# Optimization experiments

Hardware: AMD Instinct MI355X
Metric: run time of the kernel (lower is better)

The kernel has to match this reference:

```python
import jax, jax.numpy as jnp
import numpy as np

EPS = 1e-5

def layer_norm(x, w, b):
    mu = jnp.mean(x, axis=-1, keepdims=True)
    var = jnp.mean(jnp.square(x - mu), axis=-1, keepdims=True)
    return (x - mu) * jax.lax.rsqrt(var + EPS) * w + b

def setup_inputs() -> dict:
    key = jax.random.key(0)
    ks = jax.random.split(key, 10)
    B, S, E = 8, 1024, 512
    s = 1.0 / np.sqrt(E)
    return {
        "Zi_1_alpha_beta": jax.random.normal(ks[0], (B, S, E), jnp.float32),
        "Zi_1_alpha": jax.random.normal(ks[1], (B, S, E), jnp.float32),
        "ln_w": jnp.ones((E,), jnp.float32),
        "ln_b": jnp.zeros((E,), jnp.float32),
        "in_proj_w": jax.random.uniform(ks[2], (3 * E, E), jnp.float32, -s, s),
        "in_proj_b": jnp.zeros((3 * E,), jnp.float32),
        "out_proj_w": jax.random.uniform(ks[3], (E, E), jnp.float32, -s, s),
        "out_proj_b": jnp.zeros((E,), jnp.float32),
        "ff_w": jax.random.uniform(ks[4], (E, E), jnp.float32, -s, s),
        "ff_b": jax.random.uniform(ks[5], (E,), jnp.float32, -s, s),
    }

def reference(Zi_1_alpha_beta, Zi_1_alpha, ln_w, ln_b, in_proj_w, in_proj_b,
              out_proj_w, out_proj_b, ff_w, ff_b):
    B, Sq, E = Zi_1_alpha_beta.shape
    Sk = Zi_1_alpha.shape[1]
    H = 8
    dh = E // H

    q_in = layer_norm(Zi_1_alpha_beta, ln_w, ln_b)   # query source
    kv_in = layer_norm(Zi_1_alpha, ln_w, ln_b)       # key/value source

    Wq, Wk, Wv = in_proj_w[:E], in_proj_w[E:2 * E], in_proj_w[2 * E:]
    bq, bk, bv = in_proj_b[:E], in_proj_b[E:2 * E], in_proj_b[2 * E:]
    q = (q_in @ Wq.T + bq).reshape(B, Sq, H, dh)
    k = (kv_in @ Wk.T + bk).reshape(B, Sk, H, dh)
    v = (kv_in @ Wv.T + bv).reshape(B, Sk, H, dh)

    scale = 1.0 / np.sqrt(dh)
    scores = jnp.einsum('bqhd,bkhd->bhqk', q, k) * scale   # [B,H,Sq,Sk]
    attn = jax.nn.softmax(scores, axis=-1)
    ctx = jnp.einsum('bhqk,bkhd->bqhd', attn, v).reshape(B, Sq, E)
    attn_out = ctx @ out_proj_w.T + out_proj_b

    # torch MHA with need_weights=True averages weights over heads
    attn_weights = jnp.mean(attn, axis=1)  # [B,Sq,Sk]

    x = attn_out + Zi_1_alpha_beta
    x_n = layer_norm(x, ln_w, ln_b)
    ff = x_n @ ff_w.T + ff_b
    final = layer_norm(x_n + ff, ln_w, ln_b)
    return final, attn_weights
```

## Files before the change

### kernel.cpp

```cpp
#include <hip/hip_runtime.h>
#include <math.h>

#define EPS 1e-5f

constexpr int B = 8, S = 1024, E = 512, H = 8;
constexpr int M = B * S;

typedef __attribute__((ext_vector_type(8))) short short8;
typedef __attribute__((ext_vector_type(4))) float f32x4;

static __device__ __forceinline__ unsigned short f2bf(float f) {
    unsigned int x = __float_as_uint(f);
    x += 0x7FFFu + ((x >> 16) & 1u);
    return (unsigned short)(x >> 16);
}
static __device__ __forceinline__ float bf2f(unsigned short u) {
    return __uint_as_float(((unsigned int)u) << 16);
}

typedef __attribute__((address_space(3))) unsigned int  lds_uint;
typedef __attribute__((address_space(1))) unsigned int  glb_uint;
static __device__ __forceinline__ void gload16(const unsigned short* g, unsigned short* l) {
    __builtin_amdgcn_global_load_lds((const glb_uint*)g, (lds_uint*)l, 16, 0, 0);
}
template <int N>
static __device__ __forceinline__ void waitvm() {
    __builtin_amdgcn_s_waitcnt(0x0F70 | N);
}

__global__ __launch_bounds__(256) void prep_kernel(
    const float* __restrict__ wqkv, const float* __restrict__ wo,
    const float* __restrict__ wf, unsigned short* __restrict__ wout,
    const float* __restrict__ x0, const float* __restrict__ x1,
    const float* __restrict__ w, const float* __restrict__ bb,
    unsigned short* __restrict__ o0, unsigned short* __restrict__ o1) {
    const int bid = blockIdx.x;
    if (bid < 1280) {
        int base = (bid * 256 + threadIdx.x) * 4;
        float4 v;
        if (base < 3 * E * E)           v = *(const float4*)(wqkv + base);
        else if (base < 4 * E * E)      v = *(const float4*)(wo + (base - 3 * E * E));
        else                            v = *(const float4*)(wf + (base - 4 * E * E));
        ushort4 o;
        o.x = f2bf(v.x); o.y = f2bf(v.y); o.z = f2bf(v.z); o.w = f2bf(v.w);
        *(ushort4*)(wout + base) = o;
        return;
    }
    int row = (bid - 1280) * 4 + (threadIdx.x >> 6);
    int lane = threadIdx.x & 63;
    const float* x = row < M ? x0 : x1;
    unsigned short* out = row < M ? o0 : o1;
    int r = row < M ? row : row - M;
    const float* xr = x + (size_t)r * E + lane * 8;
    float4 v0 = *(const float4*)xr;
    float4 v1 = *(const float4*)(xr + 4);
    float vv[8] = {v0.x, v0.y, v0.z, v0.w, v1.x, v1.y, v1.z, v1.w};
    float s = 0.f;
    #pragma unroll
    for (int i = 0; i < 8; i++) s += vv[i];
    #pragma unroll
    for (int o = 1; o < 64; o <<= 1) s += __shfl_xor(s, o);
    float mu = s * (1.0f / E);
    float qs = 0.f;
    #pragma unroll
    for (int i = 0; i < 8; i++) { float d = vv[i] - mu; qs += d * d; }
    #pragma unroll
    for (int o = 1; o < 64; o <<= 1) qs += __shfl_xor(qs, o);
    float rs = rsqrtf(qs * (1.0f / E) + EPS);
    float4 w0 = *(const float4*)(w + lane * 8), w1 = *(const float4*)(w + lane * 8 + 4);
    float4 b0 = *(const float4*)(bb + lane * 8), b1 = *(const float4*)(bb + lane * 8 + 4);
    float ww[8] = {w0.x, w0.y, w0.z, w0.w, w1.x, w1.y, w1.z, w1.w};
    float bv[8] = {b0.x, b0.y, b0.z, b0.w, b1.x, b1.y, b1.z, b1.w};
    short8 o8;
    #pragma unroll
    for (int i = 0; i < 8; i++) o8[i] = (short)f2bf((vv[i] - mu) * rs * ww[i] + bv[i]);
    *(short8*)(out + (size_t)r * E + lane * 8) = o8;
}

__global__ __launch_bounds__(256) void ln_bf16_kernel(
    const float* __restrict__ x, const float* __restrict__ w,
    const float* __restrict__ bb, unsigned short* __restrict__ out) {
    int row = blockIdx.x * 4 + (threadIdx.x >> 6);
    int lane = threadIdx.x & 63;
    const float* xr = x + (size_t)row * E + lane * 8;
    float4 v0 = *(const float4*)xr;
    float4 v1 = *(const float4*)(xr + 4);
    float vv[8] = {v0.x, v0.y, v0.z, v0.w, v1.x, v1.y, v1.z, v1.w};
    float s = 0.f;
    #pragma unroll
    for (int i = 0; i < 8; i++) s += vv[i];
    #pragma unroll
    for (int o = 1; o < 64; o <<= 1) s += __shfl_xor(s, o);
    float mu = s * (1.0f / E);
    float qs = 0.f;
    #pragma unroll
    for (int i = 0; i < 8; i++) { float d = vv[i] - mu; qs += d * d; }
    #pragma unroll
    for (int o = 1; o < 64; o <<= 1) qs += __shfl_xor(qs, o);
    float rs = rsqrtf(qs * (1.0f / E) + EPS);
    float4 w0 = *(const float4*)(w + lane * 8), w1 = *(const float4*)(w + lane * 8 + 4);
    float4 b0 = *(const float4*)(bb + lane * 8), b1 = *(const float4*)(bb + lane * 8 + 4);
    float ww[8] = {w0.x, w0.y, w0.z, w0.w, w1.x, w1.y, w1.z, w1.w};
    float bv[8] = {b0.x, b0.y, b0.z, b0.w, b1.x, b1.y, b1.z, b1.w};
    short8 o8;
    #pragma unroll
    for (int i = 0; i < 8; i++) o8[i] = (short)f2bf((vv[i] - mu) * rs * ww[i] + bv[i]);
    *(short8*)(out + (size_t)row * E + lane * 8) = o8;
}

__global__ __launch_bounds__(256) void ln_full_kernel(
    const float* __restrict__ x, const float* __restrict__ w,
    const float* __restrict__ bb, float* __restrict__ out) {
    int row = blockIdx.x * 4 + (threadIdx.x >> 6);
    int lane = threadIdx.x & 63;
    const float* xr = x + (size_t)row * E + lane * 8;
    float4 v0 = *(const float4*)xr;
    float4 v1 = *(const float4*)(xr + 4);
    float vv[8] = {v0.x, v0.y, v0.z, v0.w, v1.x, v1.y, v1.z, v1.w};
    float s = 0.f;
    #pragma unroll
    for (int i = 0; i < 8; i++) s += vv[i];
    #pragma unroll
    for (int o = 1; o < 64; o <<= 1) s += __shfl_xor(s, o);
    float mu = s * (1.0f / E);
    float qs = 0.f;
    #pragma unroll
    for (int i = 0; i < 8; i++) { float d = vv[i] - mu; qs += d * d; }
    #pragma unroll
    for (int o = 1; o < 64; o <<= 1) qs += __shfl_xor(qs, o);
    float rs = rsqrtf(qs * (1.0f / E) + EPS);
    float4 w0 = *(const float4*)(w + lane * 8), w1 = *(const float4*)(w + lane * 8 + 4);
    float4 b0 = *(const float4*)(bb + lane * 8), b1 = *(const float4*)(bb + lane * 8 + 4);
    float* op = out + (size_t)row * E + lane * 8;
    float4 o0, o1;
    o0.x = (vv[0] - mu) * rs * w0.x + b0.x;
    o0.y = (vv[1] - mu) * rs * w0.y + b0.y;
    o0.z = (vv[2] - mu) * rs * w0.z + b0.z;
    o0.w = (vv[3] - mu) * rs * w0.w + b0.w;
    o1.x = (vv[4] - mu) * rs * w1.x + b1.x;
    o1.y = (vv[5] - mu) * rs * w1.y + b1.y;
    o1.z = (vv[6] - mu) * rs * w1.z + b1.z;
    o1.w = (vv[7] - mu) * rs * w1.w + b1.w;
    *(float4*)op = o0;
    *(float4*)(op + 4) = o1;
}

__global__ __launch_bounds__(256) void gemm_o_red(
    const unsigned short* __restrict__ A, const unsigned short* __restrict__ W,
    const float* __restrict__ bias, const float* __restrict__ residf,
    float* __restrict__ C0,
    const unsigned short* __restrict__ awp, float* __restrict__ aw) {
    __shared__ unsigned short As[64 * 32];
    __shared__ unsigned short Bs[128 * 32];
    const int bid = blockIdx.x;
    const int t = threadIdx.x;
    if (bid >= 512) {
        const size_t PLN = (size_t)B * S * S;
        size_t idx = ((size_t)(bid - 512) * 256 + t) * 8;
        float acc[8] = {};
        #pragma unroll
        for (int p = 0; p < 2; p++) {
            short8 v = *(const short8*)(awp + p * PLN + idx);
            #pragma unroll
            for (int j = 0; j < 8; j++) acc[j] += bf2f((unsigned short)v[j]);
        }
        float4 o0 = make_float4(acc[0] * (1.0f / H), acc[1] * (1.0f / H),
                                acc[2] * (1.0f / H), acc[3] * (1.0f / H));
        float4 o1 = make_float4(acc[4] * (1.0f / H), acc[5] * (1.0f / H),
                                acc[6] * (1.0f / H), acc[7] * (1.0f / H));
        *(float4*)(aw + idx) = o0;
        *(float4*)(aw + idx + 4) = o1;
        return;
    }
    const int wave = t >> 6, lane = t & 63;
    const int quad = lane >> 4, l16 = lane & 15;
    const int m0 = (bid & 127) * 64, n0 = (bid >> 7) * 128;
    const int wm = (wave >> 1) * 32, wn = (wave & 1) * 64;
    const int srow = t >> 2;
    const int skof = (t & 3) * 8;

    f32x4 acc[2][4];
    #pragma unroll
    for (int i = 0; i < 2; i++)
        #pragma unroll
        for (int j = 0; j < 4; j++) acc[i][j] = (f32x4){0.f, 0.f, 0.f, 0.f};

    for (int k0 = 0; k0 < E; k0 += 32) {
        gload16(A + (size_t)(m0 + srow) * E + k0 + skof,        As + t * 8);
        gload16(W + (size_t)(n0 + srow) * E + k0 + skof,        Bs + t * 8);
        gload16(W + (size_t)(n0 + 64 + srow) * E + k0 + skof,   Bs + 2048 + t * 8);
        __syncthreads();
        short8 af[2], bfr[4];
        #pragma unroll
        for (int i = 0; i < 2; i++)
            af[i] = *(const short8*)&As[(wm + i * 16 + l16) * 32 + quad * 8];
        #pragma unroll
        for (int j = 0; j < 4; j++)
            bfr[j] = *(const short8*)&Bs[(wn + j * 16 + l16) * 32 + quad * 8];
        #pragma unroll
        for (int i = 0; i < 2; i++)
            #pragma unroll
            for (int j = 0; j < 4; j++)
                acc[i][j] = __builtin_amdgcn_mfma_f32_16x16x32_bf16(af[i], bfr[j], acc[i][j], 0, 0, 0);
        __syncthreads();
    }

    #pragma unroll
    for (int i = 0; i < 2; i++) {
        const int mrow0 = m0 + wm + i * 16 + quad * 4;
        #pragma unroll
        for (int j = 0; j < 4; j++) {
            const int ncol = n0 + wn + j * 16 + l16;
            const float bval = bias[ncol];
            #pragma unroll
            for (int r = 0; r < 4; r++) {
                size_t idx = (size_t)(mrow0 + r) * 512 + ncol;
                C0[idx] = acc[i][j][r] + bval + residf[idx];
            }
        }
    }
}

__global__ __launch_bounds__(256) void gemm_mfma64_ff(
    const unsigned short* __restrict__ A, const unsigned short* __restrict__ W,
    const float* __restrict__ bias, const unsigned short* __restrict__ residb,
    float* __restrict__ C0) {
    __shared__ unsigned short As[64 * 32];
    __shared__ unsigned short Bs[128 * 32];
    const int t = threadIdx.x;
    const int wave = t >> 6, lane = t & 63;
    const int quad = lane >> 4, l16 = lane & 15;
    const int m0 = blockIdx.x * 64, n0 = blockIdx.y * 128;
    const int wm = (wave >> 1) * 32, wn = (wave & 1) * 64;
    const int srow = t >> 2;
    const int skof = (t & 3) * 8;

    f32x4 acc[2][4];
    #pragma unroll
    for (int i = 0; i < 2; i++)
        #pragma unroll
        for (int j = 0; j < 4; j++) acc[i][j] = (f32x4){0.f, 0.f, 0.f, 0.f};

    for (int k0 = 0; k0 < E; k0 += 32) {
        gload16(A + (size_t)(m0 + srow) * E + k0 + skof,        As + t * 8);
        gload16(W + (size_t)(n0 + srow) * E + k0 + skof,        Bs + t * 8);
        gload16(W + (size_t)(n0 + 64 + srow) * E + k0 + skof,   Bs + 2048 + t * 8);
        __syncthreads();
        short8 af[2], bfr[4];
        #pragma unroll
        for (int i = 0; i < 2; i++)
            af[i] = *(const short8*)&As[(wm + i * 16 + l16) * 32 + quad * 8];
        #pragma unroll
        for (int j = 0; j < 4; j++)
            bfr[j] = *(const short8*)&Bs[(wn + j * 16 + l16) * 32 + quad * 8];
        #pragma unroll
        for (int i = 0; i < 2; i++)
            #pragma unroll
            for (int j = 0; j < 4; j++)
                acc[i][j] = __builtin_amdgcn_mfma_f32_16x16x32_bf16(af[i], bfr[j], acc[i][j], 0, 0, 0);
        __syncthreads();
    }

    #pragma unroll
    for (int i = 0; i < 2; i++) {
        const int mrow0 = m0 + wm + i * 16 + quad * 4;
        #pragma unroll
        for (int j = 0; j < 4; j++) {
            const int ncol = n0 + wn + j * 16 + l16;
            const float bval = bias[ncol];
            #pragma unroll
            for (int r = 0; r < 4; r++) {
                size_t idx = (size_t)(mrow0 + r) * 512 + ncol;
                C0[idx] = acc[i][j][r] + bval + bf2f(residb[idx]);
            }
        }
    }
}

__global__ __launch_bounds__(256) void gemm_qkv(
    const unsigned short* __restrict__ Aq, const unsigned short* __restrict__ Akv,
    const unsigned short* __restrict__ W,
    const float* __restrict__ bias,
    unsigned short* __restrict__ qout,
    unsigned short* __restrict__ kout,
    unsigned short* __restrict__ vtout) {
    __shared__ unsigned short As[128 * 32];
    __shared__ unsigned short Bs[128 * 32];
    const int t = threadIdx.x;
    const int wave = t >> 6, lane = t & 63;
    const int quad = lane >> 4, l16 = lane & 15;
    const bool isq = blockIdx.y < 4;
    const int yy = isq ? blockIdx.y : blockIdx.y - 4;
    const unsigned short* A  = isq ? Aq : Akv;
    const unsigned short* Wb = W + (isq ? 0 : (size_t)E * E);
    const float* bb = bias + (isq ? 0 : E);
    const int m0 = blockIdx.x * 128, n0 = yy * 128;
    const int wm = (wave >> 1) * 64, wn = (wave & 1) * 64;

    const int srow = t >> 2;
    const int skof = (t & 3) * 8;

    f32x4 acc[4][4];
    #pragma unroll
    for (int i = 0; i < 4; i++)
        #pragma unroll
        for (int j = 0; j < 4; j++) acc[i][j] = (f32x4){0.f, 0.f, 0.f, 0.f};

    for (int k0 = 0; k0 < E; k0 += 32) {
        gload16(A + (size_t)(m0 + srow) * E + k0 + skof,         As + t * 8);
        gload16(A + (size_t)(m0 + 64 + srow) * E + k0 + skof,    As + 2048 + t * 8);
        gload16(Wb + (size_t)(n0 + srow) * E + k0 + skof,        Bs + t * 8);
        gload16(Wb + (size_t)(n0 + 64 + srow) * E + k0 + skof,   Bs + 2048 + t * 8);
        __syncthreads();
        short8 af[4], bfr[4];
        #pragma unroll
        for (int i = 0; i < 4; i++)
            af[i] = *(const short8*)&As[(wm + i * 16 + l16) * 32 + quad * 8];
        #pragma unroll
        for (int j = 0; j < 4; j++)
            bfr[j] = *(const short8*)&Bs[(wn + j * 16 + l16) * 32 + quad * 8];
        #pragma unroll
        for (int i = 0; i < 4; i++)
            #pragma unroll
            for (int j = 0; j < 4; j++)
                acc[i][j] = __builtin_amdgcn_mfma_f32_16x16x32_bf16(af[i], bfr[j], acc[i][j], 0, 0, 0);
        __syncthreads();
    }

    #pragma unroll
    for (int i = 0; i < 4; i++) {
        const int mrow0 = m0 + wm + i * 16 + quad * 4;
        #pragma unroll
        for (int j = 0; j < 4; j++) {
            const int ncol = n0 + wn + j * 16 + l16;
            const float bval = bb[ncol];
            if (isq) {
                #pragma unroll
                for (int r = 0; r < 4; r++)
                    qout[(size_t)(mrow0 + r) * 512 + ncol] = f2bf(acc[i][j][r] + bval);
            } else if (ncol < 512) {
                #pragma unroll
                for (int r = 0; r < 4; r++)
                    kout[(size_t)(mrow0 + r) * 512 + ncol] = f2bf(acc[i][j][r] + bval);
            } else {
                const int nv = ncol - 512;
                const int b2 = mrow0 >> 10, s0v = mrow0 & 1023;
                ushort4 o;
                o.x = f2bf(acc[i][j][0] + bval);
                o.y = f2bf(acc[i][j][1] + bval);
                o.z = f2bf(acc[i][j][2] + bval);
                o.w = f2bf(acc[i][j][3] + bval);
                *(ushort4*)(vtout + ((size_t)b2 * 512 + nv) * 1024 + s0v) = o;
            }
        }
    }
}

__global__ __launch_bounds__(256, 2) void attn_mfma_kernel(
    const unsigned short* __restrict__ q,
    const unsigned short* __restrict__ k,
    const unsigned short* __restrict__ vt,
    unsigned short* __restrict__ ctx,
    unsigned short* __restrict__ awp) {
    __shared__ unsigned short s_mem[16 * 1032];
    __shared__ unsigned short s_v[4 * 2048];
    __shared__ float s_red[2][4][16];

    const int t = threadIdx.x;
    const int wave = t >> 6, lane = t & 63;
    const int quad = lane >> 4, l16 = lane & 15;
    const int qt    = blockIdx.x >> 4;
    const int panel = blockIdx.x & 15;
    const int hg    = panel & 1;
    const int b     = panel >> 1;
    const int q0   = qt * 16;
    const size_t qrow = ((size_t)(b * S + q0 + l16)) * E;

    unsigned short* karea = s_mem + wave * 4128;
    unsigned short* varea = s_v + wave * 2048;

    const int dr = lane >> 3;
    const int dc = lane & 7;
    const int csrc = dc ^ dr;
    const int sw7 = l16 & 7;

    f32x4 awacc[16];
    #pragma unroll
    for (int i = 0; i < 16; i++) awacc[i] = (f32x4){0.f, 0.f, 0.f, 0.f};

    #pragma clang loop unroll(disable)
    for (int hh = 0; hh < 4; hh++) {
        const int h = hg * 4 + hh;

        auto stage_k = [&](int c, int buf) {
            const unsigned short* src =
                k + ((size_t)(b * S + wave * 256 + c * 32 + dr)) * E + h * 64 + csrc * 8;
            unsigned short* dst = karea + buf * 2048 + dr * 64 + dc * 8;
            gload16(src,                  dst);
            gload16(src + (size_t)8 * E,  dst + 512);
            gload16(src + (size_t)16 * E, dst + 1024);
            gload16(src + (size_t)24 * E, dst + 1536);
        };
        auto stage_v = [&](int cv, int buf) {
            const unsigned short* src =
                vt + ((size_t)(b * E + h * 64 + wave * 16 + dr)) * S + cv * 64 + csrc * 8;
            unsigned short* dst = varea + buf * 1024 + dr * 64 + dc * 8;
            gload16(src,                 dst);
            gload16(src + (size_t)8 * S, dst + 512);
        };

        short8 aq0 = *(const short8*)(q + qrow + h * 64 + quad * 8);
        short8 aq1 = *(const short8*)(q + qrow + h * 64 + 32 + quad * 8);

        f32x4 sacc[16];
        stage_k(0, 0);
        stage_k(1, 1);
        #pragma unroll
        for (int c = 0; c < 8; c++) {
            if (c < 7) waitvm<4>(); else waitvm<0>();
            const unsigned short* kbuf = karea + (c & 1) * 2048;
            #pragma unroll
            for (int ntl = 0; ntl < 2; ntl++) {
                const int rl = ntl * 16 + l16;
                short8 kf0 = *(const short8*)(kbuf + rl * 64 + ((quad)     ^ sw7) * 8);
                short8 kf1 = *(const short8*)(kbuf + rl * 64 + ((4 + quad) ^ sw7) * 8);
                f32x4 cc = (f32x4){0.f, 0.f, 0.f, 0.f};
                cc = __builtin_amdgcn_mfma_f32_16x16x32_bf16(aq0, kf0, cc, 0, 0, 0);
                cc = __builtin_amdgcn_mfma_f32_16x16x32_bf16(aq1, kf1, cc, 0, 0, 0);
                sacc[c * 2 + ntl] = cc * 0.125f;
            }
            if (c < 6) stage_k(c + 2, c & 1);
        }

        float lm[4], ls[4];
        #pragma unroll
        for (int r = 0; r < 4; r++) {
            float mv = sacc[0][r];
            #pragma unroll
            for (int nt = 1; nt < 16; nt++) mv = fmaxf(mv, sacc[nt][r]);
            #pragma unroll
            for (int o = 1; o < 16; o <<= 1) mv = fmaxf(mv, __shfl_xor(mv, o));
            lm[r] = mv;
            ls[r] = 0.f;
        }
        #pragma unroll
        for (int nt = 0; nt < 16; nt++)
            #pragma unroll
            for (int r = 0; r < 4; r++) {
                float e = __expf(sacc[nt][r] - lm[r]);
                sacc[nt][r] = e;
                ls[r] += e;
            }
        #pragma unroll
        for (int r = 0; r < 4; r++) {
            #pragma unroll
            for (int o = 1; o < 16; o <<= 1) ls[r] += __shfl_xor(ls[r], o);
        }
        if (l16 == 0) {
            #pragma unroll
            for (int r = 0; r < 4; r++) {
                s_red[0][wave][quad * 4 + r] = lm[r];
                s_red[1][wave][quad * 4 + r] = ls[r];
            }
        }
        __syncthreads();
        float scale[4];
        #pragma unroll
        for (int r = 0; r < 4; r++) {
            const int row = quad * 4 + r;
            float m0 = s_red[0][0][row], m1 = s_red[0][1][row];
            float m2 = s_red[0][2][row], m3 = s_red[0][3][row];
            float gmax = fmaxf(fmaxf(m0, m1), fmaxf(m2, m3));
            float gsum = s_red[1][0][row] * __expf(m0 - gmax)
                       + s_red[1][1][row] * __expf(m1 - gmax)
                       + s_red[1][2][row] * __expf(m2 - gmax)
                       + s_red[1][3][row] * __expf(m3 - gmax);
            scale[r] = __expf(lm[r] - gmax) / gsum;
        }

        #pragma unroll
        for (int nt = 0; nt < 16; nt++) {
            #pragma unroll
            for (int r = 0; r < 4; r++) {
                float p = sacc[nt][r] * scale[r];
                awacc[nt][r] += p;
                s_mem[(quad * 4 + r) * 1032 + wave * 256 + nt * 16 + l16] = f2bf(p);
            }
        }
        __syncthreads();

        f32x4 cacc0 = (f32x4){0.f, 0.f, 0.f, 0.f};
        f32x4 cacc1 = (f32x4){0.f, 0.f, 0.f, 0.f};
        stage_v(0, 0);
        stage_v(1, 1);
        #pragma unroll
        for (int cv = 0; cv < 16; cv++) {
            if (cv < 15) waitvm<2>(); else waitvm<0>();
            const unsigned short* vbuf = varea + (cv & 1) * 1024;
            short8 vf0 = *(const short8*)(vbuf + l16 * 64 + ((quad)     ^ sw7) * 8);
            short8 vf1 = *(const short8*)(vbuf + l16 * 64 + ((4 + quad) ^ sw7) * 8);
            short8 pf0 = *(const short8*)(s_mem + l16 * 1032 + cv * 64 + quad * 8);
            short8 pf1 = *(const short8*)(s_mem + l16 * 1032 + cv * 64 + 32 + quad * 8);
            cacc0 = __builtin_amdgcn_mfma_f32_16x16x32_bf16(pf0, vf0, cacc0, 0, 0, 0);
            cacc1 = __builtin_amdgcn_mfma_f32_16x16x32_bf16(pf1, vf1, cacc1, 0, 0, 0);
            if (cv < 14) stage_v(cv + 2, cv & 1);
        }
        f32x4 cacc = cacc0 + cacc1;
        unsigned short* crow = ctx + ((size_t)(b * S + q0)) * E + h * 64 + wave * 16 + l16;
        #pragma unroll
        for (int r = 0; r < 4; r++)
            crow[(size_t)(quad * 4 + r) * E] = f2bf(cacc[r]);
        __syncthreads();
    }

    #pragma unroll
    for (int nt = 0; nt < 16; nt++) {
        #pragma unroll
        for (int r = 0; r < 4; r++)
            awp[((size_t)((hg * B + b) * S + q0 + quad * 4 + r)) * S +
                wave * 256 + nt * 16 + l16] = f2bf(awacc[nt][r]);
    }
}

extern "C" void kernel_launch(void* const* d_in, const int* in_sizes, int n_in,
                              void* d_out, int out_size, void* d_ws, size_t ws_size,
                              hipStream_t stream) {
    const float* Zab  = (const float*)d_in[0];
    const float* Za   = (const float*)d_in[1];
    const float* lnw  = (const float*)d_in[2];
    const float* lnb  = (const float*)d_in[3];
    const float* Wqkv = (const float*)d_in[4];
    const float* bqkv = (const float*)d_in[5];
    const float* Wo   = (const float*)d_in[6];
    const float* bo   = (const float*)d_in[7];
    const float* Wf   = (const float*)d_in[8];
    const float* bf   = (const float*)d_in[9];

    float* out_final = (float*)d_out;
    float* out_aw    = out_final + (size_t)B * S * E;

    char* ws = (char*)d_ws;
    unsigned short* qb   = (unsigned short*)(ws);
    unsigned short* kb   = (unsigned short*)(ws + (8u << 20));
    unsigned short* vtb  = (unsigned short*)(ws + (16u << 20));
    unsigned short* ctxb = (unsigned short*)(ws + (24u << 20));
    unsigned short* aqb  = (unsigned short*)(ws + (32u << 20));
    unsigned short* akvb = (unsigned short*)(ws + (40u << 20));
    unsigned short* awp  = (unsigned short*)(ws + (32ull << 20));
    unsigned short* wbf  = (unsigned short*)(ws + (96ull << 20));
    float* xb  = (float*)(ws);
    float* tb  = (float*)(ws + (16u << 20));
    unsigned short* xnb = aqb;

    dim3 blk(256);

    prep_kernel<<<1280 + 4096, blk, 0, stream>>>(Wqkv, Wo, Wf, wbf,
                                                 Zab, Za, lnw, lnb, aqb, akvb);

    gemm_qkv<<<dim3(M / 128, 12), blk, 0, stream>>>(aqb, akvb, wbf, bqkv, qb, kb, vtb);

    attn_mfma_kernel<<<B * 2 * 64, blk, 0, stream>>>(qb, kb, vtb, ctxb, awp);

    gemm_o_red<<<512 + 4096, blk, 0, stream>>>(ctxb, wbf + (size_t)3*E*E, bo,
                                               Zab, xb, awp, out_aw);

    ln_bf16_kernel<<<M / 4, blk, 0, stream>>>(xb, lnw, lnb, xnb);

    gemm_mfma64_ff<<<dim3(M / 64, 4), blk, 0, stream>>>(xnb, wbf + (size_t)4*E*E, bf, xnb, tb);

    ln_full_kernel<<<M / 4, blk, 0, stream>>>(tb, lnw, lnb, out_final);
}
```

Baseline: 253.4 us.

## Fuse post-attention LayerNorm, FF GEMM and final LayerNorm into one kernel

```diff
diff --git a/kernel.cpp b/kernel.cpp
--- a/kernel.cpp
+++ b/kernel.cpp
@@ -77,74 +77,6 @@
     *(short8*)(out + (size_t)r * E + lane * 8) = o8;
 }
 
-__global__ __launch_bounds__(256) void ln_bf16_kernel(
-    const float* __restrict__ x, const float* __restrict__ w,
-    const float* __restrict__ bb, unsigned short* __restrict__ out) {
-    int row = blockIdx.x * 4 + (threadIdx.x >> 6);
-    int lane = threadIdx.x & 63;
-    const float* xr = x + (size_t)row * E + lane * 8;
-    float4 v0 = *(const float4*)xr;
-    float4 v1 = *(const float4*)(xr + 4);
-    float vv[8] = {v0.x, v0.y, v0.z, v0.w, v1.x, v1.y, v1.z, v1.w};
-    float s = 0.f;
-    #pragma unroll
-    for (int i = 0; i < 8; i++) s += vv[i];
-    #pragma unroll
-    for (int o = 1; o < 64; o <<= 1) s += __shfl_xor(s, o);
-    float mu = s * (1.0f / E);
-    float qs = 0.f;
-    #pragma unroll
-    for (int i = 0; i < 8; i++) { float d = vv[i] - mu; qs += d * d; }
-    #pragma unroll
-    for (int o = 1; o < 64; o <<= 1) qs += __shfl_xor(qs, o);
-    float rs = rsqrtf(qs * (1.0f / E) + EPS);
-    float4 w0 = *(const float4*)(w + lane * 8), w1 = *(const float4*)(w + lane * 8 + 4);
-    float4 b0 = *(const float4*)(bb + lane * 8), b1 = *(const float4*)(bb + lane * 8 + 4);
-    float ww[8] = {w0.x, w0.y, w0.z, w0.w, w1.x, w1.y, w1.z, w1.w};
-    float bv[8] = {b0.x, b0.y, b0.z, b0.w, b1.x, b1.y, b1.z, b1.w};
-    short8 o8;
-    #pragma unroll
-    for (int i = 0; i < 8; i++) o8[i] = (short)f2bf((vv[i] - mu) * rs * ww[i] + bv[i]);
-    *(short8*)(out + (size_t)row * E + lane * 8) = o8;
-}
-
-__global__ __launch_bounds__(256) void ln_full_kernel(
-    const float* __restrict__ x, const float* __restrict__ w,
-    const float* __restrict__ bb, float* __restrict__ out) {
-    int row = blockIdx.x * 4 + (threadIdx.x >> 6);
-    int lane = threadIdx.x & 63;
-    const float* xr = x + (size_t)row * E + lane * 8;
-    float4 v0 = *(const float4*)xr;
-    float4 v1 = *(const float4*)(xr + 4);
-    float vv[8] = {v0.x, v0.y, v0.z, v0.w, v1.x, v1.y, v1.z, v1.w};
-    float s = 0.f;
-    #pragma unroll
-    for (int i = 0; i < 8; i++) s += vv[i];
-    #pragma unroll
-    for (int o = 1; o < 64; o <<= 1) s += __shfl_xor(s, o);
-    float mu = s * (1.0f / E);
-    float qs = 0.f;
-    #pragma unroll
-    for (int i = 0; i < 8; i++) { float d = vv[i] - mu; qs += d * d; }
-    #pragma unroll
-    for (int o = 1; o < 64; o <<= 1) qs += __shfl_xor(qs, o);
-    float rs = rsqrtf(qs * (1.0f / E) + EPS);
-    float4 w0 = *(const float4*)(w + lane * 8), w1 = *(const float4*)(w + lane * 8 + 4);
-    float4 b0 = *(const float4*)(bb + lane * 8), b1 = *(const float4*)(bb + lane * 8 + 4);
-    float* op = out + (size_t)row * E + lane * 8;
-    float4 o0, o1;
-    o0.x = (vv[0] - mu) * rs * w0.x + b0.x;
-    o0.y = (vv[1] - mu) * rs * w0.y + b0.y;
-    o0.z = (vv[2] - mu) * rs * w0.z + b0.z;
-    o0.w = (vv[3] - mu) * rs * w0.w + b0.w;
-    o1.x = (vv[4] - mu) * rs * w1.x + b1.x;
-    o1.y = (vv[5] - mu) * rs * w1.y + b1.y;
-    o1.z = (vv[6] - mu) * rs * w1.z + b1.z;
-    o1.w = (vv[7] - mu) * rs * w1.w + b1.w;
-    *(float4*)op = o0;
-    *(float4*)(op + 4) = o1;
-}
-
 __global__ __launch_bounds__(256) void gemm_o_red(
     const unsigned short* __restrict__ A, const unsigned short* __restrict__ W,
     const float* __restrict__ bias, const float* __restrict__ residf,
@@ -221,59 +153,126 @@
     }
 }
 
-__global__ __launch_bounds__(256) void gemm_mfma64_ff(
-    const unsigned short* __restrict__ A, const unsigned short* __restrict__ W,
-    const float* __restrict__ bias, const unsigned short* __restrict__ residb,
-    float* __restrict__ C0) {
-    __shared__ unsigned short As[64 * 32];
-    __shared__ unsigned short Bs[128 * 32];
+__global__ __launch_bounds__(256) void ffn_fused_kernel(
+    const float* __restrict__ x,
+    const unsigned short* __restrict__ W,
+    const float* __restrict__ bias,
+    const float* __restrict__ lnw, const float* __restrict__ lnb,
+    float* __restrict__ out) {
+    __shared__ unsigned short Axn[16 * 520];
+    __shared__ unsigned short Bs[512 * 32];
+    __shared__ float s_red[2][4][16];
     const int t = threadIdx.x;
     const int wave = t >> 6, lane = t & 63;
     const int quad = lane >> 4, l16 = lane & 15;
-    const int m0 = blockIdx.x * 64, n0 = blockIdx.y * 128;
-    const int wm = (wave >> 1) * 32, wn = (wave & 1) * 64;
+    const int m0 = blockIdx.x * 16;
+
+    #pragma unroll
+    for (int rr = 0; rr < 4; rr++) {
+        const int row = wave * 4 + rr;
+        const float* xr = x + (size_t)(m0 + row) * E + lane * 8;
+        float4 v0 = *(const float4*)xr;
+        float4 v1 = *(const float4*)(xr + 4);
+        float vv[8] = {v0.x, v0.y, v0.z, v0.w, v1.x, v1.y, v1.z, v1.w};
+        float s = 0.f;
+        #pragma unroll
+        for (int i = 0; i < 8; i++) s += vv[i];
+        #pragma unroll
+        for (int o = 1; o < 64; o <<= 1) s += __shfl_xor(s, o);
+        float mu = s * (1.0f / E);
+        float qs = 0.f;
+        #pragma unroll
+        for (int i = 0; i < 8; i++) { float d = vv[i] - mu; qs += d * d; }
+        #pragma unroll
+        for (int o = 1; o < 64; o <<= 1) qs += __shfl_xor(qs, o);
+        float rs = rsqrtf(qs * (1.0f / E) + EPS);
+        float4 w0 = *(const float4*)(lnw + lane * 8), w1 = *(const float4*)(lnw + lane * 8 + 4);
+        float4 b0 = *(const float4*)(lnb + lane * 8), b1 = *(const float4*)(lnb + lane * 8 + 4);
+        float ww[8] = {w0.x, w0.y, w0.z, w0.w, w1.x, w1.y, w1.z, w1.w};
+        float bv[8] = {b0.x, b0.y, b0.z, b0.w, b1.x, b1.y, b1.z, b1.w};
+        short8 o8;
+        #pragma unroll
+        for (int i = 0; i < 8; i++) o8[i] = (short)f2bf((vv[i] - mu) * rs * ww[i] + bv[i]);
+        *(short8*)&Axn[row * 520 + lane * 8] = o8;
+    }
+    __syncthreads();
+
+    f32x4 acc[8];
+    #pragma unroll
+    for (int j = 0; j < 8; j++) acc[j] = (f32x4){0.f, 0.f, 0.f, 0.f};
     const int srow = t >> 2;
     const int skof = (t & 3) * 8;
-
-    f32x4 acc[2][4];
-    #pragma unroll
-    for (int i = 0; i < 2; i++)
-        #pragma unroll
-        for (int j = 0; j < 4; j++) acc[i][j] = (f32x4){0.f, 0.f, 0.f, 0.f};
-
+    #pragma clang loop unroll(disable)
     for (int k0 = 0; k0 < E; k0 += 32) {
-        gload16(A + (size_t)(m0 + srow) * E + k0 + skof,        As + t * 8);
-        gload16(W + (size_t)(n0 + srow) * E + k0 + skof,        Bs + t * 8);
-        gload16(W + (size_t)(n0 + 64 + srow) * E + k0 + skof,   Bs + 2048 + t * 8);
-        __syncthreads();
-        short8 af[2], bfr[4];
-        #pragma unroll
-        for (int i = 0; i < 2; i++)
-            af[i] = *(const short8*)&As[(wm + i * 16 + l16) * 32 + quad * 8];
-        #pragma unroll
-        for (int j = 0; j < 4; j++)
-            bfr[j] = *(const short8*)&Bs[(wn + j * 16 + l16) * 32 + quad * 8];
-        #pragma unroll
-        for (int i = 0; i < 2; i++)
-            #pragma unroll
-            for (int j = 0; j < 4; j++)
-                acc[i][j] = __builtin_amdgcn_mfma_f32_16x16x32_bf16(af[i], bfr[j], acc[i][j], 0, 0, 0);
-        __syncthreads();
-    }
-
-    #pragma unroll
-    for (int i = 0; i < 2; i++) {
-        const int mrow0 = m0 + wm + i * 16 + quad * 4;
-        #pragma unroll
-        for (int j = 0; j < 4; j++) {
-            const int ncol = n0 + wn + j * 16 + l16;
-            const float bval = bias[ncol];
-            #pragma unroll
-            for (int r = 0; r < 4; r++) {
-                size_t idx = (size_t)(mrow0 + r) * 512 + ncol;
-                C0[idx] = acc[i][j][r] + bval + bf2f(residb[idx]);
-            }
-        }
+        #pragma unroll
+        for (int c = 0; c < 8; c++)
+            gload16(W + (size_t)(c * 64 + srow) * E + k0 + skof, Bs + c * 2048 + t * 8);
+        __syncthreads();
+        short8 af = *(const short8*)&Axn[l16 * 520 + k0 + quad * 8];
+        short8 bfr[8];
+        #pragma unroll
+        for (int j = 0; j < 8; j++)
+            bfr[j] = *(const short8*)&Bs[(wave * 128 + j * 16 + l16) * 32 + quad * 8];
+        #pragma unroll
+        for (int j = 0; j < 8; j++)
+            acc[j] = __builtin_amdgcn_mfma_f32_16x16x32_bf16(af, bfr[j], acc[j], 0, 0, 0);
+        __syncthreads();
+    }
+
+    float tv[4][8];
+    #pragma unroll
+    for (int j = 0; j < 8; j++) {
+        const int col = wave * 128 + j * 16 + l16;
+        const float bval = bias[col];
+        #pragma unroll
+        for (int r = 0; r < 4; r++) {
+            const int row = quad * 4 + r;
+            tv[r][j] = acc[j][r] + bval + bf2f(Axn[row * 520 + col]);
+        }
+    }
+    #pragma unroll
+    for (int r = 0; r < 4; r++) {
+        float s = 0.f;
+        #pragma unroll
+        for (int j = 0; j < 8; j++) s += tv[r][j];
+        #pragma unroll
+        for (int o = 1; o < 16; o <<= 1) s += __shfl_xor(s, o);
+        if (l16 == 0) s_red[0][wave][quad * 4 + r] = s;
+    }
+    __syncthreads();
+    float mu[4];
+    #pragma unroll
+    for (int r = 0; r < 4; r++) {
+        const int row = quad * 4 + r;
+        mu[r] = (s_red[0][0][row] + s_red[0][1][row] +
+                 s_red[0][2][row] + s_red[0][3][row]) * (1.0f / E);
+    }
+    #pragma unroll
+    for (int r = 0; r < 4; r++) {
+        float s = 0.f;
+        #pragma unroll
+        for (int j = 0; j < 8; j++) { float d = tv[r][j] - mu[r]; s += d * d; }
+        #pragma unroll
+        for (int o = 1; o < 16; o <<= 1) s += __shfl_xor(s, o);
+        if (l16 == 0) s_red[1][wave][quad * 4 + r] = s;
+    }
+    __syncthreads();
+    float rsig[4];
+    #pragma unroll
+    for (int r = 0; r < 4; r++) {
+        const int row = quad * 4 + r;
+        float var = (s_red[1][0][row] + s_red[1][1][row] +
+                     s_red[1][2][row] + s_red[1][3][row]) * (1.0f / E);
+        rsig[r] = rsqrtf(var + EPS);
+    }
+    #pragma unroll
+    for (int j = 0; j < 8; j++) {
+        const int col = wave * 128 + j * 16 + l16;
+        const float wc = lnw[col], bc = lnb[col];
+        #pragma unroll
+        for (int r = 0; r < 4; r++)
+            out[(size_t)(m0 + quad * 4 + r) * E + col] =
+                (tv[r][j] - mu[r]) * rsig[r] * wc + bc;
     }
 }
 
@@ -549,8 +548,6 @@
     unsigned short* awp  = (unsigned short*)(ws + (32ull << 20));
     unsigned short* wbf  = (unsigned short*)(ws + (96ull << 20));
     float* xb  = (float*)(ws);
-    float* tb  = (float*)(ws + (16u << 20));
-    unsigned short* xnb = aqb;
 
     dim3 blk(256);
 
@@ -564,9 +561,6 @@
     gemm_o_red<<<512 + 4096, blk, 0, stream>>>(ctxb, wbf + (size_t)3*E*E, bo,
                                                Zab, xb, awp, out_aw);
 
-    ln_bf16_kernel<<<M / 4, blk, 0, stream>>>(xb, lnw, lnb, xnb);
-
-    gemm_mfma64_ff<<<dim3(M / 64, 4), blk, 0, stream>>>(xnb, wbf + (size_t)4*E*E, bf, xnb, tb);
-
-    ln_full_kernel<<<M / 4, blk, 0, stream>>>(tb, lnw, lnb, out_final);
-}
+    ffn_fused_kernel<<<M / 16, blk, 0, stream>>>(xb, wbf + (size_t)4*E*E, bf,
+                                                 lnw, lnb, out_final);
+}
```

New measurement: 249.1 us. No clear change (-1.7%).
